# Optimization experiments

Hardware: AMD Instinct MI355X
Metric: run time of the kernel (lower is better)

## Reference

```python
import jax, jax.numpy as jnp
import numpy as np

N_NODES = 100000
N_EDGES = 1_600_000
IN_CH = 64
HID = 128
OUT_CH = 2


def _glorot(key, shape):
    fan_in = shape[0]
    return jax.random.normal(key, shape, dtype=jnp.float32) / jnp.sqrt(jnp.float32(fan_in))


def setup_inputs() -> dict:
    key = jax.random.key(0)
    ks = jax.random.split(key, 10)
    x = jax.random.normal(ks[0], (N_NODES, IN_CH), dtype=jnp.float32)
    edge_index = jax.random.randint(ks[1], (2, N_EDGES), 0, N_NODES, dtype=jnp.int64)
    # SAGEConv layer 0: lin_l (neighbor, with bias) + lin_r (root)
    W_n0 = _glorot(ks[2], (IN_CH, HID))
    W_s0 = _glorot(ks[3], (IN_CH, HID))
    b0 = jnp.zeros((HID,), dtype=jnp.float32)
    # SAGEConv layer 1
    W_n1 = _glorot(ks[4], (HID, HID))
    W_s1 = _glorot(ks[5], (HID, HID))
    b1 = jnp.zeros((HID,), dtype=jnp.float32)
    # final fc
    fc_w = _glorot(ks[6], (HID, OUT_CH))
    fc_b = jnp.zeros((OUT_CH,), dtype=jnp.float32)
    return {"x": x, "edge_index": edge_index, "W_n0": W_n0, "W_s0": W_s0, "b0": b0,
            "W_n1": W_n1, "W_s1": W_s1, "b1": b1, "fc_w": fc_w, "fc_b": fc_b}


def _sage_conv(h, src, dst, W_n, W_s, b, num_nodes):
    # mean aggregation of source features onto destination nodes
    agg = jax.ops.segment_sum(h[src], dst, num_segments=num_nodes)  # [N, d]
    cnt = jax.ops.segment_sum(jnp.ones_like(dst, dtype=h.dtype), dst, num_segments=num_nodes)
    mean = agg / jnp.maximum(cnt, 1.0)[:, None]
    return mean @ W_n + h @ W_s + b


def reference(x, edge_index, W_n0, W_s0, b0, W_n1, W_s1, b1, fc_w, fc_b):
    src, dst = edge_index[0], edge_index[1]
    n = x.shape[0]
    h = jax.nn.relu(_sage_conv(x, src, dst, W_n0, W_s0, b0, n))  # dropout is identity in eval mode
    h = jax.nn.relu(_sage_conv(h, src, dst, W_n1, W_s1, b1, n))
    return h @ fc_w + fc_b
```

## Files before the change

### kernel.cpp

```cpp
#include <hip/hip_runtime.h>

#define N_NODES 100000
#define IN_CH 64
#define HID 128
#define NBUCK ((N_NODES + 511) >> 9)
#define NCB 256

typedef short short8 __attribute__((ext_vector_type(8)));
typedef float floatx4 __attribute__((ext_vector_type(4)));
typedef float floatx2 __attribute__((ext_vector_type(2)));

__device__ __forceinline__ unsigned short f2bf(float f) {
    unsigned u = __builtin_bit_cast(unsigned, f);
    u += 0x7fffu + ((u >> 16) & 1u);
    return (unsigned short)(u >> 16);
}

template <int K>
__device__ __forceinline__ void pack_dev(const float* __restrict__ Wn,
                                         const float* __restrict__ Ws,
                                         unsigned short* __restrict__ Bpack, int idx) {
    int s = idx >> 9;
    int rem = idx & 511;
    int t = rem >> 6;
    int lane = rem & 63;
    int quad = lane >> 4;
    int n = t * 16 + (lane & 15);
    unsigned short v[8];
#pragma unroll
    for (int j = 0; j < 8; ++j) {
        int k = s * 32 + quad * 8 + j;
        float w = (k < K) ? Wn[(size_t)k * HID + n] : Ws[(size_t)(k - K) * HID + n];
        v[j] = f2bf(w);
    }
    *(short8*)(Bpack + (size_t)idx * 8) = *(short8*)v;
}

__global__ __launch_bounds__(256) void histprep_kernel(const int* __restrict__ dst,
                                                       int* __restrict__ table, int E, int chunk,
                                                       const float* __restrict__ x,
                                                       unsigned short* __restrict__ x_bf,
                                                       unsigned char* __restrict__ x_f8,
                                                       const float* __restrict__ Wn0,
                                                       const float* __restrict__ Ws0,
                                                       unsigned short* __restrict__ Bpack0,
                                                       const float* __restrict__ Wn1,
                                                       const float* __restrict__ Ws1,
                                                       unsigned short* __restrict__ Bpack1,
                                                       int* __restrict__ scan_done, int n4) {
    int b = blockIdx.x;
    if (b < NCB) {
        if (b == 0 && threadIdx.x == 0) *scan_done = 0;
        __shared__ int h[NBUCK];
        for (int i = threadIdx.x; i < NBUCK; i += 256) h[i] = 0;
        __syncthreads();
        int e0 = b * chunk;
        int e1 = min(E, e0 + chunk);
        for (int e = e0 + threadIdx.x; e < e1; e += 256) atomicAdd(&h[dst[e] >> 9], 1);
        __syncthreads();
        for (int i = threadIdx.x; i < NBUCK; i += 256) table[i * NCB + b] = h[i];
    } else if (b < NCB + 8) {
        pack_dev<IN_CH>(Wn0, Ws0, Bpack0, (b - NCB) * 256 + threadIdx.x);
    } else if (b < NCB + 24) {
        pack_dev<HID>(Wn1, Ws1, Bpack1, (b - NCB - 8) * 256 + threadIdx.x);
    } else {
        int i = (b - NCB - 24) * 256 + threadIdx.x;
        if (i < n4) {
            float4 v = ((const float4*)x)[i];
            ushort4 o;
            o.x = f2bf(v.x); o.y = f2bf(v.y); o.z = f2bf(v.z); o.w = f2bf(v.w);
            ((ushort4*)x_bf)[i] = o;
            int p8 = __builtin_amdgcn_cvt_pk_fp8_f32(v.x, v.y, 0, false);
            p8 = __builtin_amdgcn_cvt_pk_fp8_f32(v.z, v.w, p8, true);
            ((unsigned*)x_f8)[i] = (unsigned)p8;
        }
    }
}

__global__ __launch_bounds__(256) void scan12_kernel(int* __restrict__ table,
                                                     int* __restrict__ tot,
                                                     int* __restrict__ bstart,
                                                     int* __restrict__ ptr,
                                                     int* __restrict__ scan_done, int E) {
    __shared__ int s[NCB];
    __shared__ int lastflag;
    int b = blockIdx.x, t = threadIdx.x;
    int c = table[b * NCB + t];
    s[t] = c;
    __syncthreads();
#pragma unroll
    for (int off = 1; off < NCB; off <<= 1) {
        int v = (t >= off) ? s[t - off] : 0;
        __syncthreads();
        s[t] += v;
        __syncthreads();
    }
    table[b * NCB + t] = s[t] - c;
    if (t == NCB - 1) {
        __hip_atomic_store(&tot[b], s[t], __ATOMIC_RELAXED, __HIP_MEMORY_SCOPE_AGENT);
        int prev = __hip_atomic_fetch_add(scan_done, 1, __ATOMIC_ACQ_REL, __HIP_MEMORY_SCOPE_AGENT);
        lastflag = (prev == NBUCK - 1);
    }
    __syncthreads();
    if (!lastflag) return;
    int v = (t < NBUCK) ? __hip_atomic_load(&tot[t], __ATOMIC_RELAXED, __HIP_MEMORY_SCOPE_AGENT) : 0;
    s[t] = v;
    __syncthreads();
#pragma unroll
    for (int off = 1; off < 256; off <<= 1) {
        int u = (t >= off) ? s[t - off] : 0;
        __syncthreads();
        s[t] += u;
        __syncthreads();
    }
    if (t < NBUCK) bstart[t] = s[t] - v;
    if (t == 0) {
        bstart[NBUCK] = E;
        ptr[N_NODES] = E;
    }
}

__global__ __launch_bounds__(256) void bin_kernel(const int* __restrict__ src,
                                                  const int* __restrict__ dst,
                                                  const int* __restrict__ table,
                                                  const int* __restrict__ bstart,
                                                  unsigned* __restrict__ binned, int E, int chunk) {
    __shared__ int cur[NBUCK];
    int blk = blockIdx.x;
    for (int i = threadIdx.x; i < NBUCK; i += 256) cur[i] = bstart[i] + table[i * NCB + blk];
    __syncthreads();
    int e0 = blk * chunk;
    int e1 = min(E, e0 + chunk);
    for (int e = e0 + threadIdx.x; e < e1; e += 256) {
        int d = dst[e];
        int b = d >> 9;
        int pos = atomicAdd(&cur[b], 1);
        if ((unsigned)pos < (unsigned)E)
            binned[pos] = (unsigned)src[e] | ((unsigned)(d & 511) << 17);
    }
}

__global__ __launch_bounds__(256) void place_kernel(const unsigned* __restrict__ binned,
                                                    const int* __restrict__ bstart,
                                                    int* __restrict__ ptr,
                                                    int* __restrict__ sorted, int N, int E) {
    __shared__ int deg[512];
    __shared__ int cur[512];
    __shared__ int ssum[256];
    int b = blockIdx.x, t = threadIdx.x;
    int start = bstart[b], end = bstart[b + 1];
    start = max(0, min(start, E));
    end = max(start, min(end, E));
    deg[t] = 0;
    deg[t + 256] = 0;
    __syncthreads();
    for (int i = start + t; i < end; i += 256) atomicAdd(&deg[(binned[i] >> 17) & 511], 1);
    __syncthreads();
    int a = deg[2 * t], c = deg[2 * t + 1];
    int s2 = a + c;
    ssum[t] = s2;
    __syncthreads();
#pragma unroll
    for (int off = 1; off < 256; off <<= 1) {
        int u = (t >= off) ? ssum[t - off] : 0;
        __syncthreads();
        ssum[t] += u;
        __syncthreads();
    }
    int excl2 = ssum[t] - s2;
    cur[2 * t] = excl2;
    cur[2 * t + 1] = excl2 + a;
    int n0 = b * 512 + 2 * t;
    if (n0 < N) ptr[n0] = start + excl2;
    if (n0 + 1 < N) ptr[n0 + 1] = start + excl2 + a;
    __syncthreads();
    for (int i = start + t; i < end; i += 256) {
        unsigned p = binned[i];
        int dl = (p >> 17) & 511;
        int pos = start + atomicAdd(&cur[dl], 1);
        if ((unsigned)pos < (unsigned)E) sorted[pos] = (int)(p & 0x1FFFF);
    }
}

template <int C>
__global__ __launch_bounds__(256) void gather_mean_g4p(const int* __restrict__ ptr,
                                                       const int* __restrict__ srcs,
                                                       const unsigned char* __restrict__ feat,
                                                       unsigned short* __restrict__ mean, int N,
                                                       int E) {
    constexpr int NA = C / 64;
    const int lane = threadIdx.x & 63;
    const int g = lane >> 4;
    const int l = lane & 15;
    const int w = (blockIdx.x * 4 + (threadIdx.x >> 6)) * 4 + g;
    if (w >= N) return;
    int s0 = ptr[w], s1 = ptr[w + 1];
    s0 = max(0, min(s0, E));
    s1 = max(s0, min(s1, E));
    const int deg = min(s1 - s0, 4096);

    floatx2 accq[4][2 * NA];
#pragma unroll
    for (int q = 0; q < 4; ++q)
#pragma unroll
        for (int u = 0; u < 2 * NA; ++u) { accq[q][u][0] = 0.0f; accq[q][u][1] = 0.0f; }

    const int nfull = deg & ~3;
    int j = 0;
    if (nfull > 0) {
        int cid[4];
#pragma unroll
        for (int q = 0; q < 4; ++q)
            cid[q] = (int)min((unsigned)srcs[s0 + q], (unsigned)(N_NODES - 1));
        for (; j < nfull; j += 4) {
            uint v[4][NA];
#pragma unroll
            for (int q = 0; q < 4; ++q) {
                if (NA == 2) {
                    uint2 tt = *(const uint2*)(feat + (size_t)cid[q] * C + l * 8);
                    v[q][0] = tt.x; v[q][1] = tt.y;
                } else {
                    v[q][0] = *(const unsigned*)(feat + (size_t)cid[q] * C + l * 4);
                }
            }
            int base = (j + 4 < nfull) ? s0 + j + 4 : s0;
            int cidn[4];
#pragma unroll
            for (int q = 0; q < 4; ++q)
                cidn[q] = (int)min((unsigned)srcs[base + q], (unsigned)(N_NODES - 1));
#pragma unroll
            for (int q = 0; q < 4; ++q)
#pragma unroll
                for (int a = 0; a < NA; ++a) {
                    accq[q][2 * a + 0] += __builtin_amdgcn_cvt_pk_f32_fp8(v[q][a], false);
                    accq[q][2 * a + 1] += __builtin_amdgcn_cvt_pk_f32_fp8(v[q][a], true);
                }
#pragma unroll
            for (int q = 0; q < 4; ++q) cid[q] = cidn[q];
        }
    }
    if (j < deg) {
        int cid[4];
#pragma unroll
        for (int q = 0; q < 4; ++q) {
            int jj = min(j + q, deg - 1);
            cid[q] = (int)min((unsigned)srcs[s0 + jj], (unsigned)(N_NODES - 1));
        }
        uint v[4][NA];
#pragma unroll
        for (int q = 0; q < 4; ++q) {
            if (NA == 2) {
                uint2 tt = *(const uint2*)(feat + (size_t)cid[q] * C + l * 8);
                v[q][0] = tt.x; v[q][1] = tt.y;
            } else {
                v[q][0] = *(const unsigned*)(feat + (size_t)cid[q] * C + l * 4);
            }
        }
#pragma unroll
        for (int q = 0; q < 4; ++q)
#pragma unroll
            for (int a = 0; a < NA; ++a) v[q][a] = (j + q < deg) ? v[q][a] : 0u;
#pragma unroll
        for (int q = 0; q < 4; ++q)
#pragma unroll
            for (int a = 0; a < NA; ++a) {
                accq[q][2 * a + 0] += __builtin_amdgcn_cvt_pk_f32_fp8(v[q][a], false);
                accq[q][2 * a + 1] += __builtin_amdgcn_cvt_pk_f32_fp8(v[q][a], true);
            }
    }
#pragma unroll
    for (int u = 0; u < 2 * NA; ++u) {
        accq[0][u] += accq[1][u];
        accq[2][u] += accq[3][u];
        accq[0][u] += accq[2][u];
    }
    const float inv = (deg > 0) ? 1.0f / (float)deg : 0.0f;
    unsigned short o[4 * NA];
#pragma unroll
    for (int u = 0; u < 2 * NA; ++u) {
        o[2 * u + 0] = f2bf(accq[0][u][0] * inv);
        o[2 * u + 1] = f2bf(accq[0][u][1] * inv);
    }
    if (NA == 2) *(uint4*)(mean + (size_t)w * C + l * 8) = *(const uint4*)o;
    else *(uint2*)(mean + (size_t)w * C + l * 4) = *(const uint2*)o;
}

template <int KT, bool FUSE_FC>
__global__ __launch_bounds__(256) void sage_gemm_mfma(const unsigned short* __restrict__ meanb,
                                                      const unsigned short* __restrict__ hb,
                                                      const unsigned short* __restrict__ Bpack,
                                                      const float* __restrict__ bias,
                                                      const float* __restrict__ fcw,
                                                      const float* __restrict__ fcb,
                                                      unsigned short* __restrict__ outb,
                                                      unsigned char* __restrict__ out8,
                                                      float* __restrict__ outf, int N) {
    constexpr int KH = KT / 2;
    constexpr int LDA = KT + 8;
    __shared__ unsigned short As[64 * LDA];
    const int t = threadIdx.x;
    const int row0 = blockIdx.x * 64;

    constexpr int SEGS = KT / 8;
    for (int c = t; c < 64 * SEGS; c += 256) {
        int r = c / SEGS, seg = c % SEGS;
        int rsrc = row0 + r;
        if (rsrc >= N) rsrc = N - 1;
        const unsigned short* srcp = (seg < SEGS / 2)
                                         ? meanb + (size_t)rsrc * KH + seg * 8
                                         : hb + (size_t)rsrc * KH + (seg - SEGS / 2) * 8;
        *(uint4*)&As[r * LDA + seg * 8] = *(const uint4*)srcp;
    }
    __syncthreads();

    const int lane = t & 63;
    const int wave = t >> 6;
    const int quad = lane >> 4;
    const int lo = lane & 15;

    floatx4 acc[8];
#pragma unroll
    for (int i = 0; i < 8; ++i)
#pragma unroll
        for (int r = 0; r < 4; ++r) acc[i][r] = 0.0f;

    const unsigned short* abase = &As[(wave * 16 + lo) * LDA + quad * 8];
#pragma unroll
    for (int s = 0; s < KT / 32; ++s) {
        short8 a = *(const short8*)(abase + s * 32);
        const short8* bp = (const short8*)Bpack + (size_t)(s * 8) * 64 + lane;
#pragma unroll
        for (int tt = 0; tt < 8; ++tt) {
            short8 b = bp[tt * 64];
            acc[tt] = __builtin_amdgcn_mfma_f32_16x16x32_bf16(a, b, acc[tt], 0, 0, 0);
        }
    }

    if (!FUSE_FC) {
        __syncthreads();
#pragma unroll
        for (int tt = 0; tt < 8; ++tt) {
            int col = tt * 16 + lo;
            float bv = bias[col];
#pragma unroll
            for (int r = 0; r < 4; ++r) {
                int rl = wave * 16 + quad * 4 + r;
                As[rl * LDA + col] = f2bf(fmaxf(acc[tt][r] + bv, 0.0f));
            }
        }
        __syncthreads();
        for (int i = t; i < 64 * (HID / 8); i += 256) {
            int r = i >> 4, ch = i & 15;
            int row = row0 + r;
            if (row < N)
                *(uint4*)(outb + (size_t)row * HID + ch * 8) = *(const uint4*)&As[r * LDA + ch * 8];
        }
        __syncthreads();
        unsigned char* As8 = (unsigned char*)As;
#pragma unroll
        for (int tt = 0; tt < 8; ++tt) {
            int col = tt * 16 + lo;
            float bv = bias[col];
#pragma unroll
            for (int r = 0; r < 4; ++r) {
                int rl = wave * 16 + quad * 4 + r;
                float v = fmaxf(acc[tt][r] + bv, 0.0f);
                int p8 = __builtin_amdgcn_cvt_pk_fp8_f32(v, v, 0, false);
                As8[rl * (LDA * 2) + col] = (unsigned char)(p8 & 0xff);
            }
        }
        __syncthreads();
        for (int i = t; i < 64 * (HID / 16); i += 256) {
            int r = i >> 3, ch = i & 7;
            int row = row0 + r;
            if (row < N)
                *(uint4*)(out8 + (size_t)row * HID + ch * 16) =
                    *(const uint4*)&As8[r * (LDA * 2) + ch * 16];
        }
    } else {
        float o0[4] = {}, o1[4] = {};
#pragma unroll
        for (int tt = 0; tt < 8; ++tt) {
            int col = tt * 16 + lo;
            float bv = bias[col];
            float w0 = fcw[col * 2 + 0];
            float w1 = fcw[col * 2 + 1];
#pragma unroll
            for (int r = 0; r < 4; ++r) {
                float v = fmaxf(acc[tt][r] + bv, 0.0f);
                o0[r] += v * w0;
                o1[r] += v * w1;
            }
        }
#pragma unroll
        for (int r = 0; r < 4; ++r) {
#pragma unroll
            for (int m = 8; m >= 1; m >>= 1) {
                o0[r] += __shfl_xor(o0[r], m, 16);
                o1[r] += __shfl_xor(o1[r], m, 16);
            }
        }
        if (lo == 0) {
#pragma unroll
            for (int r = 0; r < 4; ++r) {
                int row = row0 + wave * 16 + quad * 4 + r;
                if (row < N) {
                    outf[(size_t)row * 2 + 0] = o0[r] + fcb[0];
                    outf[(size_t)row * 2 + 1] = o1[r] + fcb[1];
                }
            }
        }
    }
}

extern "C" void kernel_launch(void* const* d_in, const int* in_sizes, int n_in,
                              void* d_out, int out_size, void* d_ws, size_t ws_size,
                              hipStream_t stream) {
    const float* x   = (const float*)d_in[0];
    const int*   ei  = (const int*)d_in[1];
    const float* Wn0 = (const float*)d_in[2];
    const float* Ws0 = (const float*)d_in[3];
    const float* b0  = (const float*)d_in[4];
    const float* Wn1 = (const float*)d_in[5];
    const float* Ws1 = (const float*)d_in[6];
    const float* b1  = (const float*)d_in[7];
    const float* fcw = (const float*)d_in[8];
    const float* fcb = (const float*)d_in[9];
    float* out = (float*)d_out;

    const int E = in_sizes[1] / 2;
    const int* src = ei;
    const int* dst = ei + E;
    const int N = N_NODES;
    const int chunk = (E + NCB - 1) / NCB;

    char* ws = (char*)d_ws;
    size_t off = 0;
    int* table  = (int*)(ws + off); off += (size_t)NBUCK * NCB * 4;
    int* tot    = (int*)(ws + off); off += 4096;
    int* bstart = (int*)(ws + off); off += 4096;
    int* scan_done = (int*)(ws + off); off += 256;
    int* ptr    = (int*)(ws + off); off += (size_t)(N + 1) * 4 + 60; off &= ~(size_t)63;
    unsigned* binned = (unsigned*)(ws + off); off += (size_t)E * 4;
    int* sorted = (int*)(ws + off); off += (size_t)E * 4;
    off = (off + 255) & ~(size_t)255;
    unsigned short* x_bf   = (unsigned short*)(ws + off); off += (size_t)N * IN_CH * 2;
    unsigned short* mean0  = (unsigned short*)(ws + off); off += (size_t)N * IN_CH * 2;
    unsigned short* h1_bf  = (unsigned short*)(ws + off); off += (size_t)N * HID * 2;
    unsigned short* mean1  = (unsigned short*)(ws + off); off += (size_t)N * HID * 2;
    unsigned char*  h1_f8  = (unsigned char*)(ws + off);  off += (size_t)N * HID;
    unsigned char*  x_f8   = (unsigned char*)(ws + off);  off += (size_t)N * IN_CH;
    off = (off + 255) & ~(size_t)255;
    unsigned short* Bpack0 = (unsigned short*)(ws + off); off += (size_t)(2 * IN_CH / 32) * 8 * 64 * 8 * 2;
    unsigned short* Bpack1 = (unsigned short*)(ws + off); off += (size_t)(2 * HID / 32) * 8 * 64 * 8 * 2;

    {
        int n4 = N * IN_CH / 4;
        int nblk = NCB + 24 + (n4 + 255) / 256;
        histprep_kernel<<<nblk, 256, 0, stream>>>(dst, table, E, chunk, x, x_bf, x_f8,
                                                  Wn0, Ws0, Bpack0, Wn1, Ws1, Bpack1,
                                                  scan_done, n4);
    }
    scan12_kernel<<<NBUCK, 256, 0, stream>>>(table, tot, bstart, ptr, scan_done, E);
    bin_kernel<<<NCB, 256, 0, stream>>>(src, dst, table, bstart, binned, E, chunk);
    place_kernel<<<NBUCK, 256, 0, stream>>>(binned, bstart, ptr, sorted, N, E);

    const int gblk = (N + 15) / 16;
    gather_mean_g4p<IN_CH><<<gblk, 256, 0, stream>>>(ptr, sorted, x_f8, mean0, N, E);
    sage_gemm_mfma<2 * IN_CH, false><<<(N + 63) / 64, 256, 0, stream>>>(
        mean0, x_bf, Bpack0, b0, nullptr, nullptr, h1_bf, h1_f8, nullptr, N);

    gather_mean_g4p<HID><<<gblk, 256, 0, stream>>>(ptr, sorted, h1_f8, mean1, N, E);
    sage_gemm_mfma<2 * HID, true><<<(N + 63) / 64, 256, 0, stream>>>(
        mean1, h1_bf, Bpack1, b1, fcw, fcb, nullptr, nullptr, out, N);
}
```

Baseline: 240.5 us.

## Fuse CSR scan, bin and place kernels into one persistent kernel with grid barriers

After: 301.2 us. 25.2% more time.

```diff
diff --git a/kernel.cpp b/kernel.cpp
--- a/kernel.cpp
+++ b/kernel.cpp
@@ -47,10 +47,10 @@
                                                        const float* __restrict__ Wn1,
                                                        const float* __restrict__ Ws1,
                                                        unsigned short* __restrict__ Bpack1,
-                                                       int* __restrict__ scan_done, int n4) {
+                                                       int* __restrict__ bar, int n4) {
     int b = blockIdx.x;
     if (b < NCB) {
-        if (b == 0 && threadIdx.x == 0) *scan_done = 0;
+        if (b == 0 && threadIdx.x < 4) bar[threadIdx.x] = 0;
         __shared__ int h[NBUCK];
         for (int i = threadIdx.x; i < NBUCK; i += 256) h[i] = 0;
         __syncthreads();
@@ -77,108 +77,119 @@
     }
 }
 
-__global__ __launch_bounds__(256) void scan12_kernel(int* __restrict__ table,
-                                                     int* __restrict__ tot,
-                                                     int* __restrict__ bstart,
-                                                     int* __restrict__ ptr,
-                                                     int* __restrict__ scan_done, int E) {
-    __shared__ int s[NCB];
-    __shared__ int lastflag;
-    int b = blockIdx.x, t = threadIdx.x;
-    int c = table[b * NCB + t];
-    s[t] = c;
+__device__ __forceinline__ void gbar(int* __restrict__ bar, int phase) {
     __syncthreads();
-#pragma unroll
-    for (int off = 1; off < NCB; off <<= 1) {
-        int v = (t >= off) ? s[t - off] : 0;
-        __syncthreads();
-        s[t] += v;
-        __syncthreads();
-    }
-    table[b * NCB + t] = s[t] - c;
-    if (t == NCB - 1) {
-        __hip_atomic_store(&tot[b], s[t], __ATOMIC_RELAXED, __HIP_MEMORY_SCOPE_AGENT);
-        int prev = __hip_atomic_fetch_add(scan_done, 1, __ATOMIC_ACQ_REL, __HIP_MEMORY_SCOPE_AGENT);
-        lastflag = (prev == NBUCK - 1);
+    if (threadIdx.x == 0) {
+        __threadfence();
+        __hip_atomic_fetch_add(&bar[phase], 1, __ATOMIC_ACQ_REL, __HIP_MEMORY_SCOPE_AGENT);
+        int spins = 0;
+        while (__hip_atomic_load(&bar[phase], __ATOMIC_RELAXED, __HIP_MEMORY_SCOPE_AGENT) < NCB) {
+            if (++spins > (1 << 22)) break;
+        }
+        __threadfence();
     }
     __syncthreads();
-    if (!lastflag) return;
-    int v = (t < NBUCK) ? __hip_atomic_load(&tot[t], __ATOMIC_RELAXED, __HIP_MEMORY_SCOPE_AGENT) : 0;
-    s[t] = v;
-    __syncthreads();
-#pragma unroll
-    for (int off = 1; off < 256; off <<= 1) {
-        int u = (t >= off) ? s[t - off] : 0;
-        __syncthreads();
-        s[t] += u;
-        __syncthreads();
-    }
-    if (t < NBUCK) bstart[t] = s[t] - v;
-    if (t == 0) {
-        bstart[NBUCK] = E;
-        ptr[N_NODES] = E;
-    }
-}
-
-__global__ __launch_bounds__(256) void bin_kernel(const int* __restrict__ src,
-                                                  const int* __restrict__ dst,
-                                                  const int* __restrict__ table,
-                                                  const int* __restrict__ bstart,
-                                                  unsigned* __restrict__ binned, int E, int chunk) {
-    __shared__ int cur[NBUCK];
-    int blk = blockIdx.x;
-    for (int i = threadIdx.x; i < NBUCK; i += 256) cur[i] = bstart[i] + table[i * NCB + blk];
-    __syncthreads();
-    int e0 = blk * chunk;
-    int e1 = min(E, e0 + chunk);
-    for (int e = e0 + threadIdx.x; e < e1; e += 256) {
-        int d = dst[e];
-        int b = d >> 9;
-        int pos = atomicAdd(&cur[b], 1);
-        if ((unsigned)pos < (unsigned)E)
-            binned[pos] = (unsigned)src[e] | ((unsigned)(d & 511) << 17);
-    }
-}
-
-__global__ __launch_bounds__(256) void place_kernel(const unsigned* __restrict__ binned,
-                                                    const int* __restrict__ bstart,
-                                                    int* __restrict__ ptr,
-                                                    int* __restrict__ sorted, int N, int E) {
-    __shared__ int deg[512];
-    __shared__ int cur[512];
-    __shared__ int ssum[256];
-    int b = blockIdx.x, t = threadIdx.x;
-    int start = bstart[b], end = bstart[b + 1];
-    start = max(0, min(start, E));
-    end = max(start, min(end, E));
-    deg[t] = 0;
-    deg[t + 256] = 0;
-    __syncthreads();
-    for (int i = start + t; i < end; i += 256) atomicAdd(&deg[(binned[i] >> 17) & 511], 1);
-    __syncthreads();
-    int a = deg[2 * t], c = deg[2 * t + 1];
-    int s2 = a + c;
-    ssum[t] = s2;
-    __syncthreads();
-#pragma unroll
-    for (int off = 1; off < 256; off <<= 1) {
-        int u = (t >= off) ? ssum[t - off] : 0;
-        __syncthreads();
-        ssum[t] += u;
-        __syncthreads();
-    }
-    int excl2 = ssum[t] - s2;
-    cur[2 * t] = excl2;
-    cur[2 * t + 1] = excl2 + a;
-    int n0 = b * 512 + 2 * t;
-    if (n0 < N) ptr[n0] = start + excl2;
-    if (n0 + 1 < N) ptr[n0 + 1] = start + excl2 + a;
-    __syncthreads();
-    for (int i = start + t; i < end; i += 256) {
-        unsigned p = binned[i];
-        int dl = (p >> 17) & 511;
-        int pos = start + atomicAdd(&cur[dl], 1);
-        if ((unsigned)pos < (unsigned)E) sorted[pos] = (int)(p & 0x1FFFF);
+}
+
+__global__ __launch_bounds__(256) void csr_fused(int* __restrict__ table,
+                                                 int* __restrict__ tot,
+                                                 int* __restrict__ bstart,
+                                                 int* __restrict__ ptr,
+                                                 const int* __restrict__ src,
+                                                 const int* __restrict__ dst,
+                                                 unsigned* __restrict__ binned,
+                                                 int* __restrict__ sorted,
+                                                 int* __restrict__ bar,
+                                                 int N, int E, int chunk) {
+    __shared__ int smem[1280];
+    const int b = blockIdx.x, t = threadIdx.x;
+
+    if (b < NBUCK) {
+        int c = table[b * NCB + t];
+        smem[t] = c;
+        __syncthreads();
+#pragma unroll
+        for (int off = 1; off < NCB; off <<= 1) {
+            int v = (t >= off) ? smem[t - off] : 0;
+            __syncthreads();
+            smem[t] += v;
+            __syncthreads();
+        }
+        table[b * NCB + t] = smem[t] - c;
+        if (t == NCB - 1) tot[b] = smem[t];
+    }
+    gbar(bar, 0);
+
+    if (b == 0) {
+        int v = (t < NBUCK) ? tot[t] : 0;
+        smem[t] = v;
+        __syncthreads();
+#pragma unroll
+        for (int off = 1; off < 256; off <<= 1) {
+            int u = (t >= off) ? smem[t - off] : 0;
+            __syncthreads();
+            smem[t] += u;
+            __syncthreads();
+        }
+        if (t < NBUCK) bstart[t] = smem[t] - v;
+        if (t == 0) {
+            bstart[NBUCK] = E;
+            ptr[N] = E;
+        }
+    }
+    gbar(bar, 1);
+
+    {
+        for (int i = t; i < NBUCK; i += 256) smem[i] = bstart[i] + table[i * NCB + b];
+        __syncthreads();
+        int e0 = b * chunk;
+        int e1 = min(E, e0 + chunk);
+        for (int e = e0 + t; e < e1; e += 256) {
+            int d = dst[e];
+            int bk = d >> 9;
+            int pos = atomicAdd(&smem[bk], 1);
+            if ((unsigned)pos < (unsigned)E)
+                binned[pos] = (unsigned)src[e] | ((unsigned)(d & 511) << 17);
+        }
+    }
+    gbar(bar, 2);
+
+    if (b < NBUCK) {
+        int* deg = smem;
+        int* cur = smem + 512;
+        int* ssum = smem + 1024;
+        int start = bstart[b], end = bstart[b + 1];
+        start = max(0, min(start, E));
+        end = max(start, min(end, E));
+        deg[t] = 0;
+        deg[t + 256] = 0;
+        __syncthreads();
+        for (int i = start + t; i < end; i += 256) atomicAdd(&deg[(binned[i] >> 17) & 511], 1);
+        __syncthreads();
+        int a = deg[2 * t], c2 = deg[2 * t + 1];
+        int s2 = a + c2;
+        ssum[t] = s2;
+        __syncthreads();
+#pragma unroll
+        for (int off = 1; off < 256; off <<= 1) {
+            int u = (t >= off) ? ssum[t - off] : 0;
+            __syncthreads();
+            ssum[t] += u;
+            __syncthreads();
+        }
+        int excl2 = ssum[t] - s2;
+        cur[2 * t] = excl2;
+        cur[2 * t + 1] = excl2 + a;
+        int n0 = b * 512 + 2 * t;
+        if (n0 < N) ptr[n0] = start + excl2;
+        if (n0 + 1 < N) ptr[n0 + 1] = start + excl2 + a;
+        __syncthreads();
+        for (int i = start + t; i < end; i += 256) {
+            unsigned p = binned[i];
+            int dl = (p >> 17) & 511;
+            int pos = start + atomicAdd(&cur[dl], 1);
+            if ((unsigned)pos < (unsigned)E) sorted[pos] = (int)(p & 0x1FFFF);
+        }
     }
 }
 
@@ -439,7 +450,7 @@
     int* table  = (int*)(ws + off); off += (size_t)NBUCK * NCB * 4;
     int* tot    = (int*)(ws + off); off += 4096;
     int* bstart = (int*)(ws + off); off += 4096;
-    int* scan_done = (int*)(ws + off); off += 256;
+    int* bar    = (int*)(ws + off); off += 256;
     int* ptr    = (int*)(ws + off); off += (size_t)(N + 1) * 4 + 60; off &= ~(size_t)63;
     unsigned* binned = (unsigned*)(ws + off); off += (size_t)E * 4;
     int* sorted = (int*)(ws + off); off += (size_t)E * 4;
@@ -459,11 +470,10 @@
         int nblk = NCB + 24 + (n4 + 255) / 256;
         histprep_kernel<<<nblk, 256, 0, stream>>>(dst, table, E, chunk, x, x_bf, x_f8,
                                                   Wn0, Ws0, Bpack0, Wn1, Ws1, Bpack1,
-                                                  scan_done, n4);
-    }
-    scan12_kernel<<<NBUCK, 256, 0, stream>>>(table, tot, bstart, ptr, scan_done, E);
-    bin_kernel<<<NCB, 256, 0, stream>>>(src, dst, table, bstart, binned, E, chunk);
-    place_kernel<<<NBUCK, 256, 0, stream>>>(binned, bstart, ptr, sorted, N, E);
+                                                  bar, n4);
+    }
+    csr_fused<<<NCB, 256, 0, stream>>>(table, tot, bstart, ptr, src, dst, binned, sorted,
+                                       bar, N, E, chunk);
 
     const int gblk = (N + 15) / 16;
     gather_mean_g4p<IN_CH><<<gblk, 256, 0, stream>>>(ptr, sorted, x_f8, mean0, N, E);
```
